# Kernel tuning notes

Measured on AMD Instinct MI355X. Metric: run time of the kernel, lower is better.

Reference implementation:

```python
import jax, jax.numpy as jnp
import numpy as np

VOC_SIZE = 100000
EMB_SIZE = 300
BATCH = 262144


def setup_inputs() -> dict:
    key = jax.random.key(0)
    k1, k2, k3, k4, k5, k6, k7, k8 = jax.random.split(key, 8)
    center = jax.random.randint(k1, (BATCH, 1), 0, VOC_SIZE)
    outside = jax.random.randint(k2, (BATCH, 1), 0, VOC_SIZE)
    coocs = jax.random.uniform(k3, (BATCH, 1), dtype=jnp.float32)
    weighting = jax.random.uniform(k4, (BATCH, 1), dtype=jnp.float32)
    center_embedding = jax.random.normal(k5, (VOC_SIZE, EMB_SIZE), dtype=jnp.float32)
    outside_embedding = jax.random.normal(k6, (VOC_SIZE, EMB_SIZE), dtype=jnp.float32)
    center_bias = jax.random.normal(k7, (VOC_SIZE, 1), dtype=jnp.float32)
    outside_bias = jax.random.normal(k8, (VOC_SIZE, 1), dtype=jnp.float32)
    return {
        "center": center,
        "outside": outside,
        "coocs": coocs,
        "weighting": weighting,
        "center_embedding": center_embedding,
        "outside_embedding": outside_embedding,
        "center_bias": center_bias,
        "outside_bias": outside_bias,
    }


def reference(center, outside, coocs, weighting,
              center_embedding, outside_embedding,
              center_bias, outside_bias):
    c_idx = center[:, 0]    # [B]
    o_idx = outside[:, 0]   # [B]
    center_embeds = center_embedding[c_idx]     # [B, E]
    outside_embeds = outside_embedding[o_idx]   # [B, E]
    c_bias = center_bias[c_idx]                 # [B, 1]
    o_bias = outside_bias[o_idx]                # [B, 1]
    # per-sample dot product, keepdims to match [B, 1]
    inner = jnp.sum(center_embeds * outside_embeds, axis=-1, keepdims=True)  # [B, 1]
    err = inner + c_bias + o_bias - coocs
    loss = jnp.sum(weighting * err * err)
    return loss
```

## Files before the change

kernel.cpp:

```cpp
#include <hip/hip_runtime.h>

#define BATCH 262144
#define EMB 300
#define NBLK 4096
#define WPB 4
#define PPW 16

__global__ __launch_bounds__(256) void glove_main(
    const int*   __restrict__ center,
    const int*   __restrict__ outside,
    const float* __restrict__ coocs,
    const float* __restrict__ weighting,
    const float* __restrict__ cemb,
    const float* __restrict__ oemb,
    const float* __restrict__ cbias,
    const float* __restrict__ obias,
    float*       __restrict__ block_sums)
{
    const int lane = threadIdx.x & 63;
    const int warp = threadIdx.x >> 6;
    const int base = (blockIdx.x * WPB + warp) * PPW;

    int ci[PPW], oi[PPW];
    #pragma unroll
    for (int j = 0; j < PPW; ++j) {
        ci[j] = center[base + j];
        oi[j] = outside[base + j];
    }

    float acc[PPW];
    #pragma unroll
    for (int j = 0; j < PPW; ++j) {
        const float4* __restrict__ A = (const float4*)(cemb + (long)ci[j] * EMB);
        const float4* __restrict__ B = (const float4*)(oemb + (long)oi[j] * EMB);
        float4 a = A[lane];
        float4 b = B[lane];
        float s = a.x * b.x + a.y * b.y + a.z * b.z + a.w * b.w;
        if (lane < 11) {
            float4 a2 = A[lane + 64];
            float4 b2 = B[lane + 64];
            s += a2.x * b2.x + a2.y * b2.y + a2.z * b2.z + a2.w * b2.w;
        }
        acc[j] = s;
    }

    float cb[PPW], ob2[PPW], cc[PPW], wt[PPW];
    #pragma unroll
    for (int j = 0; j < PPW; ++j) {
        cc[j]  = coocs[base + j];
        wt[j]  = weighting[base + j];
        cb[j]  = cbias[ci[j]];
        ob2[j] = obias[oi[j]];
    }

    #pragma unroll
    for (int off = 32; off > 0; off >>= 1) {
        #pragma unroll
        for (int j = 0; j < PPW; ++j)
            acc[j] += __shfl_down(acc[j], off, 64);
    }

    float local = 0.0f;
    if (lane == 0) {
        #pragma unroll
        for (int j = 0; j < PPW; ++j) {
            const float e = acc[j] + cb[j] + ob2[j] - cc[j];
            local += wt[j] * e * e;
        }
    }

    __shared__ float smem[WPB];
    if (lane == 0) smem[warp] = local;
    __syncthreads();
    if (threadIdx.x == 0)
        block_sums[blockIdx.x] = smem[0] + smem[1] + smem[2] + smem[3];
}

__global__ __launch_bounds__(1024) void glove_reduce(
    const float* __restrict__ part, float* __restrict__ out)
{
    const int t = threadIdx.x;
    float4 v = ((const float4*)part)[t];
    float s = v.x + v.y + v.z + v.w;
    #pragma unroll
    for (int off = 32; off > 0; off >>= 1)
        s += __shfl_down(s, off, 64);
    __shared__ float sm[16];
    if ((t & 63) == 0) sm[t >> 6] = s;
    __syncthreads();
    if (t < 16) {
        float x = sm[t];
        #pragma unroll
        for (int off = 8; off > 0; off >>= 1)
            x += __shfl_down(x, off, 16);
        if (t == 0) out[0] = x;
    }
}

extern "C" void kernel_launch(void* const* d_in, const int* in_sizes, int n_in,
                              void* d_out, int out_size, void* d_ws, size_t ws_size,
                              hipStream_t stream) {
    const int*   center    = (const int*)  d_in[0];
    const int*   outside   = (const int*)  d_in[1];
    const float* coocs     = (const float*)d_in[2];
    const float* weighting = (const float*)d_in[3];
    const float* cemb      = (const float*)d_in[4];
    const float* oemb      = (const float*)d_in[5];
    const float* cbias     = (const float*)d_in[6];
    const float* obias     = (const float*)d_in[7];
    float* out        = (float*)d_out;
    float* block_sums = (float*)d_ws;

    glove_main<<<NBLK, 256, 0, stream>>>(
        center, outside, coocs, weighting, cemb, oemb, cbias, obias, block_sums);
    glove_reduce<<<1, 1024, 0, stream>>>(block_sums, out);
}
```

Baseline: 316.0 us.

## Split wavefront into 16-lane groups with double-buffered row prefetch

Each 64-lane wavefront becomes four 16-lane groups, and each group handles one sample per iteration, so a wavefront covers 4 samples at a time instead of one. Each lane loads up to five float4s per row, and the dot-product reduction needs only four xor shuffles. The next sample's embedding rows, biases, coocs and weights are prefetched into a second register buffer while the current one is reduced, to overlap gather latency with compute. This raises register use, which may lower occupancy, and fewer loads are in flight per thread compared with the fully unrolled 16-sample loop.

```diff
diff --git a/kernel.cpp b/kernel.cpp
--- a/kernel.cpp
+++ b/kernel.cpp
@@ -4,7 +4,6 @@
 #define EMB 300
 #define NBLK 4096
 #define WPB 4
-#define PPW 16
 
 __global__ __launch_bounds__(256) void glove_main(
     const int*   __restrict__ center,
@@ -17,62 +16,98 @@
     const float* __restrict__ obias,
     float*       __restrict__ block_sums)
 {
-    const int lane = threadIdx.x & 63;
-    const int warp = threadIdx.x >> 6;
-    const int base = (blockIdx.x * WPB + warp) * PPW;
+    const int tid  = threadIdx.x;
+    const int warp = tid >> 6;
+    const int lane = tid & 63;
+    const int l    = lane & 15;
+    const int g    = lane >> 4;
+    const int base = (blockIdx.x * WPB + warp) * 16 + g;
 
-    int ci[PPW], oi[PPW];
+    int ci[4], oi[4];
     #pragma unroll
-    for (int j = 0; j < PPW; ++j) {
-        ci[j] = center[base + j];
-        oi[j] = outside[base + j];
+    for (int it = 0; it < 4; ++it) {
+        ci[it] = center[base + it * 4];
+        oi[it] = outside[base + it * 4];
     }
 
-    float acc[PPW];
-    #pragma unroll
-    for (int j = 0; j < PPW; ++j) {
-        const float4* __restrict__ A = (const float4*)(cemb + (long)ci[j] * EMB);
-        const float4* __restrict__ B = (const float4*)(oemb + (long)oi[j] * EMB);
-        float4 a = A[lane];
-        float4 b = B[lane];
-        float s = a.x * b.x + a.y * b.y + a.z * b.z + a.w * b.w;
-        if (lane < 11) {
-            float4 a2 = A[lane + 64];
-            float4 b2 = B[lane + 64];
-            s += a2.x * b2.x + a2.y * b2.y + a2.z * b2.z + a2.w * b2.w;
-        }
-        acc[j] = s;
-    }
-
-    float cb[PPW], ob2[PPW], cc[PPW], wt[PPW];
-    #pragma unroll
-    for (int j = 0; j < PPW; ++j) {
-        cc[j]  = coocs[base + j];
-        wt[j]  = weighting[base + j];
-        cb[j]  = cbias[ci[j]];
-        ob2[j] = obias[oi[j]];
-    }
+    float4 sa[2][5], sb[2][5];
+    float  scb[2], sob[2], scc[2], swt[2];
 
     #pragma unroll
-    for (int off = 32; off > 0; off >>= 1) {
+    for (int s = 0; s < 2; ++s) {
+        const float4* __restrict__ A = (const float4*)(cemb + (long)ci[s] * EMB);
+        const float4* __restrict__ B = (const float4*)(oemb + (long)oi[s] * EMB);
         #pragma unroll
-        for (int j = 0; j < PPW; ++j)
-            acc[j] += __shfl_down(acc[j], off, 64);
+        for (int i = 0; i < 4; ++i) {
+            sa[s][i] = A[i * 16 + l];
+            sb[s][i] = B[i * 16 + l];
+        }
+        sa[s][4].x = 0.f; sa[s][4].y = 0.f; sa[s][4].z = 0.f; sa[s][4].w = 0.f;
+        sb[s][4] = sa[s][4];
+        if (l < 11) {
+            sa[s][4] = A[64 + l];
+            sb[s][4] = B[64 + l];
+        }
+        scb[s] = cbias[ci[s]];
+        sob[s] = obias[oi[s]];
+        scc[s] = coocs[base + s * 4];
+        swt[s] = weighting[base + s * 4];
     }
 
     float local = 0.0f;
-    if (lane == 0) {
+
+    #pragma unroll
+    for (int it = 0; it < 4; ++it) {
+        const int buf = it & 1;
+
+        float s = 0.f;
         #pragma unroll
-        for (int j = 0; j < PPW; ++j) {
-            const float e = acc[j] + cb[j] + ob2[j] - cc[j];
-            local += wt[j] * e * e;
+        for (int i = 0; i < 5; ++i) {
+            s += sa[buf][i].x * sb[buf][i].x + sa[buf][i].y * sb[buf][i].y
+               + sa[buf][i].z * sb[buf][i].z + sa[buf][i].w * sb[buf][i].w;
+        }
+        const float cbv = scb[buf], obv = sob[buf], ccv = scc[buf], wtv = swt[buf];
+
+        if (it + 2 < 4) {
+            const int n = it + 2;
+            const float4* __restrict__ A = (const float4*)(cemb + (long)ci[n] * EMB);
+            const float4* __restrict__ B = (const float4*)(oemb + (long)oi[n] * EMB);
+            #pragma unroll
+            for (int i = 0; i < 4; ++i) {
+                sa[buf][i] = A[i * 16 + l];
+                sb[buf][i] = B[i * 16 + l];
+            }
+            if (l < 11) {
+                sa[buf][4] = A[64 + l];
+                sb[buf][4] = B[64 + l];
+            } else {
+                sa[buf][4].x = 0.f; sa[buf][4].y = 0.f; sa[buf][4].z = 0.f; sa[buf][4].w = 0.f;
+                sb[buf][4] = sa[buf][4];
+            }
+            scb[buf] = cbias[ci[n]];
+            sob[buf] = obias[oi[n]];
+            scc[buf] = coocs[base + n * 4];
+            swt[buf] = weighting[base + n * 4];
+        }
+
+        s += __shfl_xor(s, 1);
+        s += __shfl_xor(s, 2);
+        s += __shfl_xor(s, 4);
+        s += __shfl_xor(s, 8);
+
+        if (l == 0) {
+            const float e = s + cbv + obv - ccv;
+            local += wtv * e * e;
         }
     }
+
+    local += __shfl_down(local, 32, 64);
+    local += __shfl_down(local, 16, 64);
 
     __shared__ float smem[WPB];
     if (lane == 0) smem[warp] = local;
     __syncthreads();
-    if (threadIdx.x == 0)
+    if (tid == 0)
         block_sums[blockIdx.x] = smem[0] + smem[1] + smem[2] + smem[3];
 }
 
```

Measured after the change: 304.5 us. -3.6%, faster.

## Assign four lanes per sample instead of one wavefront per sample

Applied to the files above, without the earlier changes.

Remaps the work so each group of 4 lanes handles one sample and each lane loops over 18-19 float4 chunks of the embedding rows, replacing the layout where a whole 64-lane wavefront covered one sample. The per-sample 64-lane shuffle reduction becomes a 2-step xor shuffle, followed by one wavefront reduction of the weighted errors. The aim is to cut shuffle and reduction overhead and the idle lanes in the tail chunk. The cost is that each lane's loads now stride 64 bytes apart within a row, so coalescing changes, and per-lane register use rises.

```diff
diff --git a/kernel.cpp b/kernel.cpp
--- a/kernel.cpp
+++ b/kernel.cpp
@@ -3,8 +3,6 @@
 #define BATCH 262144
 #define EMB 300
 #define NBLK 4096
-#define WPB 4
-#define PPW 16
 
 __global__ __launch_bounds__(256) void glove_main(
     const int*   __restrict__ center,
@@ -17,62 +15,50 @@
     const float* __restrict__ obias,
     float*       __restrict__ block_sums)
 {
-    const int lane = threadIdx.x & 63;
-    const int warp = threadIdx.x >> 6;
-    const int base = (blockIdx.x * WPB + warp) * PPW;
+    const int tid  = threadIdx.x;
+    const int warp = tid >> 6;
+    const int lane = tid & 63;
+    const int l4   = lane & 3;
+    const int pg   = lane >> 2;
+    const int p    = (blockIdx.x * 4 + warp) * 16 + pg;
 
-    int ci[PPW], oi[PPW];
+    const int   ci = center[p];
+    const int   oi = outside[p];
+    const float cc = coocs[p];
+    const float wt = weighting[p];
+    const float cb = cbias[ci];
+    const float ob = obias[oi];
+
+    const float4* __restrict__ A = (const float4*)(cemb + (long)ci * EMB);
+    const float4* __restrict__ B = (const float4*)(oemb + (long)oi * EMB);
+
+    float acc = 0.0f;
     #pragma unroll
-    for (int j = 0; j < PPW; ++j) {
-        ci[j] = center[base + j];
-        oi[j] = outside[base + j];
+    for (int k = 0; k < 18; ++k) {
+        float4 a = A[l4 + 4 * k];
+        float4 b = B[l4 + 4 * k];
+        acc += a.x * b.x + a.y * b.y + a.z * b.z + a.w * b.w;
+    }
+    if (l4 < 3) {
+        float4 a = A[72 + l4];
+        float4 b = B[72 + l4];
+        acc += a.x * b.x + a.y * b.y + a.z * b.z + a.w * b.w;
     }
 
-    float acc[PPW];
-    #pragma unroll
-    for (int j = 0; j < PPW; ++j) {
-        const float4* __restrict__ A = (const float4*)(cemb + (long)ci[j] * EMB);
-        const float4* __restrict__ B = (const float4*)(oemb + (long)oi[j] * EMB);
-        float4 a = A[lane];
-        float4 b = B[lane];
-        float s = a.x * b.x + a.y * b.y + a.z * b.z + a.w * b.w;
-        if (lane < 11) {
-            float4 a2 = A[lane + 64];
-            float4 b2 = B[lane + 64];
-            s += a2.x * b2.x + a2.y * b2.y + a2.z * b2.z + a2.w * b2.w;
-        }
-        acc[j] = s;
-    }
+    acc += __shfl_xor(acc, 1);
+    acc += __shfl_xor(acc, 2);
 
-    float cb[PPW], ob2[PPW], cc[PPW], wt[PPW];
-    #pragma unroll
-    for (int j = 0; j < PPW; ++j) {
-        cc[j]  = coocs[base + j];
-        wt[j]  = weighting[base + j];
-        cb[j]  = cbias[ci[j]];
-        ob2[j] = obias[oi[j]];
-    }
+    const float e = acc + cb + ob - cc;
+    float local = (l4 == 0) ? wt * e * e : 0.0f;
 
     #pragma unroll
-    for (int off = 32; off > 0; off >>= 1) {
-        #pragma unroll
-        for (int j = 0; j < PPW; ++j)
-            acc[j] += __shfl_down(acc[j], off, 64);
-    }
+    for (int off = 32; off > 0; off >>= 1)
+        local += __shfl_down(local, off, 64);
 
-    float local = 0.0f;
-    if (lane == 0) {
-        #pragma unroll
-        for (int j = 0; j < PPW; ++j) {
-            const float e = acc[j] + cb[j] + ob2[j] - cc[j];
-            local += wt[j] * e * e;
-        }
-    }
-
-    __shared__ float smem[WPB];
+    __shared__ float smem[4];
     if (lane == 0) smem[warp] = local;
     __syncthreads();
-    if (threadIdx.x == 0)
+    if (tid == 0)
         block_sums[blockIdx.x] = smem[0] + smem[1] + smem[2] + smem[3];
 }
 
```

After: 311.1 us. No clear change (-1.5%).
